# Kernel tuning notes

Measured on AMD Instinct MI355X. Metric: run time of the kernel, lower is better.

Reference implementation:

```python
import jax, jax.numpy as jnp
import numpy as np

IN_DIM = 1024
OUT_DIM = 1024
NUM_EXPERTS = 8
TOP_K = 2
B = 8192


def setup_inputs() -> dict:
    key = jax.random.key(0)
    ks = jax.random.split(key, 8)
    s_in = 1.0 / np.sqrt(IN_DIM)
    s_out = 1.0 / np.sqrt(OUT_DIM)
    return {
        "x": jax.random.normal(ks[0], (B, IN_DIM), dtype=jnp.float32),
        # router Linear(in_dim, num_experts)
        "rw": jax.random.uniform(ks[1], (IN_DIM, NUM_EXPERTS), jnp.float32, -s_in, s_in),
        "rb": jax.random.uniform(ks[2], (NUM_EXPERTS,), jnp.float32, -s_in, s_in),
        # expert MLPs stacked along expert axis
        "w1": jax.random.uniform(ks[3], (NUM_EXPERTS, IN_DIM, OUT_DIM), jnp.float32, -s_in, s_in),
        "b1": jax.random.uniform(ks[4], (NUM_EXPERTS, OUT_DIM), jnp.float32, -s_in, s_in),
        "w2": jax.random.uniform(ks[5], (NUM_EXPERTS, OUT_DIM, OUT_DIM), jnp.float32, -s_out, s_out),
        "b2": jax.random.uniform(ks[6], (NUM_EXPERTS, OUT_DIM), jnp.float32, -s_out, s_out),
    }


def reference(x, rw, rb, w1, b1, w2, b2):
    # ---- TopkRouter ----
    logits = x @ rw + rb                                  # [B, E]
    topk_vals, topk_idx = jax.lax.top_k(logits, TOP_K)    # [B, K]
    neg_inf = jnp.full_like(logits, -jnp.inf)
    rows = jnp.arange(logits.shape[0])[:, None]
    sparse_logits = neg_inf.at[rows, topk_idx].set(topk_vals)
    gating = jax.nn.softmax(sparse_logits, axis=-1)       # zeros outside top-k

    # ---- experts: dense compute, gating weights are exactly 0 for
    # non-selected experts so the weighted combine matches the masked
    # dispatch of the original module. ----
    h = jax.nn.relu(jnp.einsum('bi,eio->beo', x, w1) + b1[None])   # [B, E, out]
    y = jnp.einsum('beh,eho->beo', h, w2) + b2[None]               # [B, E, out]
    fused = jnp.einsum('beo,be->bo', y, gating)                    # [B, out]
    return fused, gating
```

## Files before the change

kernel.cpp:

```cpp
#include <hip/hip_runtime.h>
#include <hip/hip_bf16.h>
#include <cstdint>
#include <cstddef>

#define IN_DIM 1024
#define OUT_DIM 1024
#define NE 8
#define NTOK 8192
#define MT_TILES 20

typedef __bf16 bf16x8 __attribute__((ext_vector_type(8)));
typedef float f32x4 __attribute__((ext_vector_type(4)));
typedef unsigned short ushort8v __attribute__((ext_vector_type(8)));

__device__ __forceinline__ unsigned short f2bf(float f) {
    unsigned u = __float_as_uint(f);
    unsigned r = 0x7fffu + ((u >> 16) & 1u);
    return (unsigned short)((u + r) >> 16);
}

__device__ __forceinline__ void bf2x(unsigned u, float& lo, float& hi) {
    lo = __uint_as_float(u << 16);
    hi = __uint_as_float(u & 0xffff0000u);
}

__device__ __forceinline__ void async16(void* lds, const void* g) {
    __builtin_amdgcn_global_load_lds(
        (const __attribute__((address_space(1))) unsigned int*)g,
        (__attribute__((address_space(3))) unsigned int*)lds,
        16, 0, 0);
}

__global__ __launch_bounds__(256) void convert_transpose_kernel(
    const float* __restrict__ w1, const float* __restrict__ w2,
    unsigned short* __restrict__ w1T, unsigned short* __restrict__ w2T) {
    __shared__ float tile[64][69];
    int z = blockIdx.z;
    const float* src = (z < 8) ? (w1 + (size_t)z * IN_DIM * OUT_DIM)
                               : (w2 + (size_t)(z - 8) * OUT_DIM * OUT_DIM);
    unsigned short* dst = (z < 8) ? (w1T + (size_t)z * IN_DIM * OUT_DIM)
                                  : (w2T + (size_t)(z - 8) * OUT_DIM * OUT_DIM);
    int kt = blockIdx.x * 64, nt = blockIdx.y * 64;
    int t = threadIdx.x;
    int r = t >> 2, cq = (t & 3) * 16;
#pragma unroll
    for (int q = 0; q < 4; ++q) {
        float4 v = *(const float4*)(src + (size_t)(kt + r) * 1024 + nt + cq + q * 4);
        tile[r][cq + q * 4 + 0] = v.x;
        tile[r][cq + q * 4 + 1] = v.y;
        tile[r][cq + q * 4 + 2] = v.z;
        tile[r][cq + q * 4 + 3] = v.w;
    }
    __syncthreads();
    int n2 = t >> 3, k8 = (t & 7) * 8;
#pragma unroll
    for (int q = 0; q < 2; ++q) {
        int n = n2 + q * 32;
        ushort8v o;
#pragma unroll
        for (int i = 0; i < 8; ++i) o[i] = f2bf(tile[k8 + i][n]);
        *(ushort8v*)(dst + (size_t)(nt + n) * 1024 + kt + k8) = o;
    }
}

__global__ __launch_bounds__(256) void router_kernel(
    const float* __restrict__ x, const float* __restrict__ rw,
    const float* __restrict__ rb,
    unsigned short* __restrict__ xb,
    float* __restrict__ gating, int* __restrict__ enc,
    float2* __restrict__ gw, int* __restrict__ cnt) {
    __shared__ float srw[NE * IN_DIM];
    int t = threadIdx.x;
    if (blockIdx.x == 0 && t < NE) cnt[t] = 0;
#pragma unroll
    for (int i = 0; i < 4; ++i) {
        int k = t + i * 256;
        float4 a = *(const float4*)(rw + (size_t)k * NE);
        float4 b = *(const float4*)(rw + (size_t)k * NE + 4);
        srw[0 * IN_DIM + k] = a.x; srw[1 * IN_DIM + k] = a.y;
        srw[2 * IN_DIM + k] = a.z; srw[3 * IN_DIM + k] = a.w;
        srw[4 * IN_DIM + k] = b.x; srw[5 * IN_DIM + k] = b.y;
        srw[6 * IN_DIM + k] = b.z; srw[7 * IN_DIM + k] = b.w;
    }
    __syncthreads();
    int wave = t >> 6, lane = t & 63;
    int tok = blockIdx.x * 4 + wave;
    const float* xrow = x + (size_t)tok * IN_DIM;
    unsigned short* xbrow = xb + (size_t)tok * IN_DIM;
    float acc[NE] = {0, 0, 0, 0, 0, 0, 0, 0};
#pragma unroll
    for (int i = 0; i < 4; ++i) {
        int k = i * 256 + lane * 4;
        float4 xv = *(const float4*)(xrow + k);
        ushort4 o;
        o.x = f2bf(xv.x); o.y = f2bf(xv.y); o.z = f2bf(xv.z); o.w = f2bf(xv.w);
        *(ushort4*)(xbrow + k) = o;
#pragma unroll
        for (int e = 0; e < NE; ++e) {
            float4 wv = *(const float4*)(srw + e * IN_DIM + k);
            acc[e] = fmaf(xv.x, wv.x, fmaf(xv.y, wv.y, fmaf(xv.z, wv.z, fmaf(xv.w, wv.w, acc[e]))));
        }
    }
#pragma unroll
    for (int e = 0; e < NE; ++e) {
#pragma unroll
        for (int off = 32; off > 0; off >>= 1) acc[e] += __shfl_xor(acc[e], off);
        acc[e] += rb[e];
    }
    int e0 = 0; float v0 = acc[0];
#pragma unroll
    for (int e = 1; e < NE; ++e) if (acc[e] > v0) { v0 = acc[e]; e0 = e; }
    int e1 = -1; float v1 = -3.4e38f;
#pragma unroll
    for (int e = 0; e < NE; ++e) if (e != e0 && acc[e] > v1) { v1 = acc[e]; e1 = e; }
    float tg = __expf(v1 - v0);
    float inv = 1.0f / (1.0f + tg);
    float g0 = inv, g1 = tg * inv;
    if (lane < NE) gating[(size_t)tok * NE + lane] = (lane == e0) ? g0 : ((lane == e1) ? g1 : 0.0f);
    if (lane == 0) {
        enc[tok] = e0 | (e1 << 8);
        gw[tok] = make_float2(g0, g1);
    }
}

__global__ __launch_bounds__(256) void bucket_kernel(
    const int* __restrict__ enc,
    int* __restrict__ bidx, int* __restrict__ slots, int* __restrict__ cnt) {
    int tok = blockIdx.x * 256 + threadIdx.x;
    int lane = threadIdx.x & 63;
    int v = enc[tok];
    int e0 = v & 0xff, e1 = (v >> 8) & 0xff;
    unsigned long long below = (1ull << lane) - 1ull;
    int p0 = 0, p1 = 0;
#pragma unroll
    for (int e = 0; e < NE; ++e) {
        unsigned long long m0 = __ballot(e0 == e);
        unsigned long long m1 = __ballot(e1 == e);
        int c0 = __popcll(m0), c1 = __popcll(m1);
        int base = 0;
        if (lane == 0 && (c0 + c1)) base = atomicAdd(&cnt[e], c0 + c1);
        base = __shfl(base, 0);
        if (e0 == e) p0 = base + __popcll(m0 & below);
        if (e1 == e) p1 = base + c0 + __popcll(m1 & below);
    }
    bidx[e0 * NTOK + p0] = tok;
    bidx[e1 * NTOK + p1] = tok;
    slots[2 * tok + 0] = (e0 << 13) | p0;
    slots[2 * tok + 1] = (e1 << 13) | p1;
}

__device__ __forceinline__ int prefix_cnt(const int* __restrict__ cnt, int e) {
    int s = 0;
    for (int i = 0; i < NE; ++i) s += (i < e) ? cnt[i] : 0;
    return s;
}

__device__ __forceinline__ void kstep(const unsigned short* Ab,
                                      const unsigned short* Bb,
                                      f32x4 (&acc)[4][4], int wm, int wn,
                                      int lhalf, int slot) {
    bf16x8 av[4], bv[4];
#pragma unroll
    for (int i = 0; i < 4; ++i)
        av[i] = *(const bf16x8*)(Ab + (wm * 32 + i * 8 + lhalf) * 64 + slot);
#pragma unroll
    for (int j = 0; j < 4; ++j)
        bv[j] = *(const bf16x8*)(Bb + (wn * 32 + j * 8 + lhalf) * 64 + slot);
#pragma unroll
    for (int i = 0; i < 4; ++i)
#pragma unroll
        for (int j = 0; j < 4; ++j)
            acc[i][j] = __builtin_amdgcn_mfma_f32_16x16x32_bf16(av[i], bv[j], acc[i][j], 0, 0, 0);
}


__global__ __launch_bounds__(256) void gemm1_kernel(
    const unsigned short* __restrict__ xb, const unsigned short* __restrict__ w1T,
    const float* __restrict__ b1, const int* __restrict__ bidx,
    const int* __restrict__ cnt,
    unsigned short* __restrict__ H) {
    int b = blockIdx.x;
    int e = b & 7;
    int t2 = b >> 3;
    int nt = t2 & 7;
    int mt = t2 >> 3;
    int n_e = cnt[e];
    if (mt * 128 >= n_e) return;
    __shared__ __attribute__((aligned(16))) unsigned short As[3][64 * 64];
    __shared__ __attribute__((aligned(16))) unsigned short Bs[3][64 * 64];
    int t = threadIdx.x, wave = t >> 6, lane = t & 63;
    const int* be = bidx + e * NTOK;
    const unsigned short* agp[2]; const unsigned short* bgp[2];
    int ldsoff[2];
#pragma unroll
    for (int is = 0; is < 2; ++is) {
        int c = is * 256 + t;
        int line = c >> 3;
        int chunkg = (c & 7) ^ (line & 7);
        int sub = chunkg >> 2;
        int growl = 2 * line + sub;
        int growlB = (line >> 5) * 64 + (line & 7) * 8 + sub * 4 + ((line >> 3) & 3);
        int gcol = (chunkg & 3) * 8;
        int gra = mt * 128 + growl;
        int grac = gra < n_e ? gra : n_e - 1;
        agp[is] = xb + (size_t)be[grac] * IN_DIM + gcol;
        bgp[is] = w1T + ((size_t)e * OUT_DIM + nt * 128 + growlB) * IN_DIM + gcol;
        ldsoff[is] = (is * 256 + wave * 64) * 8;
    }
    int wm = wave & 1, wn = wave >> 1;
    int quad = lane >> 4, l15 = lane & 15;
    int lhalf = l15 >> 1;
    int slot = (((l15 & 1) * 4 + quad) ^ lhalf) * 8;
    f32x4 zero4 = {0.f, 0.f, 0.f, 0.f};
    f32x4 acc[4][4];
#pragma unroll
    for (int i = 0; i < 4; ++i)
#pragma unroll
        for (int j = 0; j < 4; ++j) acc[i][j] = zero4;

#pragma unroll
    for (int pt = 0; pt < 2; ++pt)
#pragma unroll
        for (int is = 0; is < 2; ++is) {
            async16(&As[pt][ldsoff[is]], agp[is] + pt * 32);
            async16(&Bs[pt][ldsoff[is]], bgp[is] + pt * 32);
        }
    int cb = 0, sb = 2;
    for (int it = 0; it < 31; ++it) {
        asm volatile("s_waitcnt vmcnt(4)\n\ts_barrier" ::: "memory");
        if (it < 30) {
            int ktn = (it + 2) * 32;
#pragma unroll
            for (int is = 0; is < 2; ++is) {
                async16(&As[sb][ldsoff[is]], agp[is] + ktn);
                async16(&Bs[sb][ldsoff[is]], bgp[is] + ktn);
            }
        }
        kstep(As[cb], Bs[cb], acc, wm, wn, lhalf, slot);
        cb = (cb == 2) ? 0 : cb + 1;
        sb = (sb == 2) ? 0 : sb + 1;
    }
    asm volatile("s_waitcnt vmcnt(0)\n\ts_barrier" ::: "memory");
    kstep(As[cb], Bs[cb], acc, wm, wn, lhalf, slot);

    int hbase = prefix_cnt(cnt, e);
    const float* b1e = b1 + (size_t)e * OUT_DIM;
    int n0 = nt * 128 + wn * 64 + l15 * 4;
    float4 bias = *(const float4*)(b1e + n0);
#pragma unroll
    for (int i = 0; i < 4; ++i) {
        int m0 = mt * 128 + wm * 64 + i * 16 + quad * 4;
#pragma unroll
        for (int r = 0; r < 4; ++r) {
            int gm = m0 + r;
            if (gm < n_e) {
                float h0 = acc[i][0][r] + bias.x; h0 = h0 > 0.f ? h0 : 0.f;
                float h1 = acc[i][1][r] + bias.y; h1 = h1 > 0.f ? h1 : 0.f;
                float h2 = acc[i][2][r] + bias.z; h2 = h2 > 0.f ? h2 : 0.f;
                float h3 = acc[i][3][r] + bias.w; h3 = h3 > 0.f ? h3 : 0.f;
                ushort4 o;
                o.x = f2bf(h0); o.y = f2bf(h1); o.z = f2bf(h2); o.w = f2bf(h3);
                *(ushort4*)(H + (size_t)(hbase + gm) * OUT_DIM + n0) = o;
            }
        }
    }
}

__global__ __launch_bounds__(256) void gemm2_kernel(
    const unsigned short* __restrict__ H, const unsigned short* __restrict__ w2T,
    const int* __restrict__ cnt,
    unsigned short* __restrict__ Y) {
    int b = blockIdx.x;
    int e = b & 7;
    int t2 = b >> 3;
    int nt = t2 & 7;
    int mt = t2 >> 3;
    int n_e = cnt[e];
    if (mt * 128 >= n_e) return;
    __shared__ __attribute__((aligned(16))) unsigned short As[3][64 * 64];
    __shared__ __attribute__((aligned(16))) unsigned short Bs[3][64 * 64];
    int t = threadIdx.x, wave = t >> 6, lane = t & 63;
    int hbase = prefix_cnt(cnt, e);
    const unsigned short* agp[2]; const unsigned short* bgp[2];
    int ldsoff[2];
#pragma unroll
    for (int is = 0; is < 2; ++is) {
        int c = is * 256 + t;
        int line = c >> 3;
        int chunkg = (c & 7) ^ (line & 7);
        int sub = chunkg >> 2;
        int growl = 2 * line + sub;
        int growlB = (line >> 5) * 64 + (line & 7) * 8 + sub * 4 + ((line >> 3) & 3);
        int gcol = (chunkg & 3) * 8;
        int gra = mt * 128 + growl;
        int grac = gra < n_e ? gra : n_e - 1;
        agp[is] = H + (size_t)(hbase + grac) * OUT_DIM + gcol;
        bgp[is] = w2T + ((size_t)e * OUT_DIM + nt * 128 + growlB) * OUT_DIM + gcol;
        ldsoff[is] = (is * 256 + wave * 64) * 8;
    }
    int wm = wave & 1, wn = wave >> 1;
    int quad = lane >> 4, l15 = lane & 15;
    int lhalf = l15 >> 1;
    int slot = (((l15 & 1) * 4 + quad) ^ lhalf) * 8;
    f32x4 zero4 = {0.f, 0.f, 0.f, 0.f};
    f32x4 acc[4][4];
#pragma unroll
    for (int i = 0; i < 4; ++i)
#pragma unroll
        for (int j = 0; j < 4; ++j) acc[i][j] = zero4;

#pragma unroll
    for (int pt = 0; pt < 2; ++pt)
#pragma unroll
        for (int is = 0; is < 2; ++is) {
            async16(&As[pt][ldsoff[is]], agp[is] + pt * 32);
            async16(&Bs[pt][ldsoff[is]], bgp[is] + pt * 32);
        }
    int cb = 0, sb = 2;
    for (int it = 0; it < 31; ++it) {
        asm volatile("s_waitcnt vmcnt(4)\n\ts_barrier" ::: "memory");
        if (it < 30) {
            int ktn = (it + 2) * 32;
#pragma unroll
            for (int is = 0; is < 2; ++is) {
                async16(&As[sb][ldsoff[is]], agp[is] + ktn);
                async16(&Bs[sb][ldsoff[is]], bgp[is] + ktn);
            }
        }
        kstep(As[cb], Bs[cb], acc, wm, wn, lhalf, slot);
        cb = (cb == 2) ? 0 : cb + 1;
        sb = (sb == 2) ? 0 : sb + 1;
    }
    asm volatile("s_waitcnt vmcnt(0)\n\ts_barrier" ::: "memory");
    kstep(As[cb], Bs[cb], acc, wm, wn, lhalf, slot);

    int n0 = nt * 128 + wn * 64 + l15 * 4;
#pragma unroll
    for (int i = 0; i < 4; ++i) {
        int m0 = mt * 128 + wm * 64 + i * 16 + quad * 4;
#pragma unroll
        for (int r = 0; r < 4; ++r) {
            int gm = m0 + r;
            if (gm < n_e) {
                ushort4 o;
                o.x = f2bf(acc[i][0][r]); o.y = f2bf(acc[i][1][r]);
                o.z = f2bf(acc[i][2][r]); o.w = f2bf(acc[i][3][r]);
                *(ushort4*)(Y + (size_t)(hbase + gm) * OUT_DIM + n0) = o;
            }
        }
    }
}

__global__ __launch_bounds__(256) void combine_kernel(
    const unsigned short* __restrict__ Y, const float* __restrict__ b2,
    const float2* __restrict__ gw, const int* __restrict__ slots,
    const int* __restrict__ cnt, float* __restrict__ out) {
    int t = threadIdx.x, wave = t >> 6, lane = t & 63;
    int tok = blockIdx.x * 4 + wave;
    int pre[NE];
    {
        int s = 0;
#pragma unroll
        for (int i = 0; i < NE; ++i) { pre[i] = s; s += cnt[i]; }
    }
    int s0 = slots[2 * tok], s1 = slots[2 * tok + 1];
    int e0 = s0 >> 13, e1 = s1 >> 13;
    int r0 = pre[e0] + (s0 & 8191);
    int r1 = pre[e1] + (s1 & 8191);
    float2 g = gw[tok];
    const unsigned short* y0 = Y + (size_t)r0 * OUT_DIM;
    const unsigned short* y1 = Y + (size_t)r1 * OUT_DIM;
    const float* c0 = b2 + (size_t)e0 * OUT_DIM;
    const float* c1 = b2 + (size_t)e1 * OUT_DIM;
    float* orow = out + (size_t)tok * OUT_DIM;
#pragma unroll
    for (int i = 0; i < 2; ++i) {
        int c = i * 512 + lane * 8;
        uint4 ua = *(const uint4*)(y0 + c);
        uint4 ub = *(const uint4*)(y1 + c);
        float a[8], b[8];
        bf2x(ua.x, a[0], a[1]); bf2x(ua.y, a[2], a[3]);
        bf2x(ua.z, a[4], a[5]); bf2x(ua.w, a[6], a[7]);
        bf2x(ub.x, b[0], b[1]); bf2x(ub.y, b[2], b[3]);
        bf2x(ub.z, b[4], b[5]); bf2x(ub.w, b[6], b[7]);
        float4 p0 = *(const float4*)(c0 + c);
        float4 p1 = *(const float4*)(c0 + c + 4);
        float4 q0 = *(const float4*)(c1 + c);
        float4 q1 = *(const float4*)(c1 + c + 4);
        float o[8];
        o[0] = g.x * (a[0] + p0.x) + g.y * (b[0] + q0.x);
        o[1] = g.x * (a[1] + p0.y) + g.y * (b[1] + q0.y);
        o[2] = g.x * (a[2] + p0.z) + g.y * (b[2] + q0.z);
        o[3] = g.x * (a[3] + p0.w) + g.y * (b[3] + q0.w);
        o[4] = g.x * (a[4] + p1.x) + g.y * (b[4] + q1.x);
        o[5] = g.x * (a[5] + p1.y) + g.y * (b[5] + q1.y);
        o[6] = g.x * (a[6] + p1.z) + g.y * (b[6] + q1.z);
        o[7] = g.x * (a[7] + p1.w) + g.y * (b[7] + q1.w);
        *(float4*)(orow + c) = make_float4(o[0], o[1], o[2], o[3]);
        *(float4*)(orow + c + 4) = make_float4(o[4], o[5], o[6], o[7]);
    }
}

extern "C" void kernel_launch(void* const* d_in, const int* in_sizes, int n_in,
                              void* d_out, int out_size, void* d_ws, size_t ws_size,
                              hipStream_t stream) {
    const float* x  = (const float*)d_in[0];
    const float* rw = (const float*)d_in[1];
    const float* rb = (const float*)d_in[2];
    const float* w1 = (const float*)d_in[3];
    const float* b1 = (const float*)d_in[4];
    const float* w2 = (const float*)d_in[5];
    const float* b2 = (const float*)d_in[6];
    float* out = (float*)d_out;
    float* gating = out + (size_t)NTOK * OUT_DIM;

    char* ws = (char*)d_ws;
    unsigned short* xb  = (unsigned short*)(ws + 0);
    unsigned short* Y   = (unsigned short*)(ws + 0);
    unsigned short* w1T = (unsigned short*)(ws + 16777216);
    unsigned short* w2T = (unsigned short*)(ws + 33554432);
    unsigned short* H   = (unsigned short*)(ws + 50331648);
    int*   bidx  = (int*)(ws + 83886080);
    int*   slots = (int*)(ws + 84148224);
    int*   cnt   = (int*)(ws + 84213760);
    int*    enc  = (int*)(ws + 84213888);
    float2* gw   = (float2*)(ws + 84246656);

    convert_transpose_kernel<<<dim3(16, 16, 16), 256, 0, stream>>>(w1, w2, w1T, w2T);
    router_kernel<<<NTOK / 4, 256, 0, stream>>>(x, rw, rb, xb, gating, enc, gw, cnt);
    bucket_kernel<<<NTOK / 256, 256, 0, stream>>>(enc, bidx, slots, cnt);
    gemm1_kernel<<<8 * 8 * MT_TILES, 256, 0, stream>>>(xb, w1T, b1, bidx, cnt, H);
    gemm2_kernel<<<8 * 8 * MT_TILES, 256, 0, stream>>>(H, w2T, cnt, Y);
    combine_kernel<<<NTOK / 4, 256, 0, stream>>>(Y, b2, gw, slots, cnt, out);
    (void)in_sizes; (void)n_in; (void)out_size; (void)ws_size;
}
```

Baseline: 294.6 us.

## Fuse combine into gemm2 epilogue via gated atomic adds to output

Removes the separate combine kernel and the bf16 Y intermediate. The gemm2 epilogue now adds bias, multiplies by the gate weight, and atomically accumulates straight into the zeroed fp32 output. Each bidx entry carries a flag bit telling which of the token's two gate weights applies. This drops the Y write and re-read plus one launch, but adds a memset of the output and 2x scattered scalar fp32 atomics, which can be slow and make the summation order nondeterministic.

```diff
diff --git a/kernel.cpp b/kernel.cpp
--- a/kernel.cpp
+++ b/kernel.cpp
@@ -17,11 +17,6 @@
     unsigned u = __float_as_uint(f);
     unsigned r = 0x7fffu + ((u >> 16) & 1u);
     return (unsigned short)((u + r) >> 16);
-}
-
-__device__ __forceinline__ void bf2x(unsigned u, float& lo, float& hi) {
-    lo = __uint_as_float(u << 16);
-    hi = __uint_as_float(u & 0xffff0000u);
 }
 
 __device__ __forceinline__ void async16(void* lds, const void* g) {
@@ -125,7 +120,7 @@
 
 __global__ __launch_bounds__(256) void bucket_kernel(
     const int* __restrict__ enc,
-    int* __restrict__ bidx, int* __restrict__ slots, int* __restrict__ cnt) {
+    int* __restrict__ bidx, int* __restrict__ cnt) {
     int tok = blockIdx.x * 256 + threadIdx.x;
     int lane = threadIdx.x & 63;
     int v = enc[tok];
@@ -144,9 +139,7 @@
         if (e1 == e) p1 = base + c0 + __popcll(m1 & below);
     }
     bidx[e0 * NTOK + p0] = tok;
-    bidx[e1 * NTOK + p1] = tok;
-    slots[2 * tok + 0] = (e0 << 13) | p0;
-    slots[2 * tok + 1] = (e1 << 13) | p1;
+    bidx[e1 * NTOK + p1] = tok | 0x8000;
 }
 
 __device__ __forceinline__ int prefix_cnt(const int* __restrict__ cnt, int e) {
@@ -203,7 +196,7 @@
         int gcol = (chunkg & 3) * 8;
         int gra = mt * 128 + growl;
         int grac = gra < n_e ? gra : n_e - 1;
-        agp[is] = xb + (size_t)be[grac] * IN_DIM + gcol;
+        agp[is] = xb + (size_t)(be[grac] & 0x7fff) * IN_DIM + gcol;
         bgp[is] = w1T + ((size_t)e * OUT_DIM + nt * 128 + growlB) * IN_DIM + gcol;
         ldsoff[is] = (is * 256 + wave * 64) * 8;
     }
@@ -268,8 +261,9 @@
 
 __global__ __launch_bounds__(256) void gemm2_kernel(
     const unsigned short* __restrict__ H, const unsigned short* __restrict__ w2T,
-    const int* __restrict__ cnt,
-    unsigned short* __restrict__ Y) {
+    const float* __restrict__ b2, const int* __restrict__ bidx,
+    const float2* __restrict__ gw, const int* __restrict__ cnt,
+    float* __restrict__ out) {
     int b = blockIdx.x;
     int e = b & 7;
     int t2 = b >> 3;
@@ -335,6 +329,9 @@
     kstep(As[cb], Bs[cb], acc, wm, wn, lhalf, slot);
 
     int n0 = nt * 128 + wn * 64 + l15 * 4;
+    const float* b2e = b2 + (size_t)e * OUT_DIM;
+    float4 bias = *(const float4*)(b2e + n0);
+    const int* be = bidx + e * NTOK;
 #pragma unroll
     for (int i = 0; i < 4; ++i) {
         int m0 = mt * 128 + wm * 64 + i * 16 + quad * 4;
@@ -342,62 +339,17 @@
         for (int r = 0; r < 4; ++r) {
             int gm = m0 + r;
             if (gm < n_e) {
-                ushort4 o;
-                o.x = f2bf(acc[i][0][r]); o.y = f2bf(acc[i][1][r]);
-                o.z = f2bf(acc[i][2][r]); o.w = f2bf(acc[i][3][r]);
-                *(ushort4*)(Y + (size_t)(hbase + gm) * OUT_DIM + n0) = o;
+                int v = be[gm];
+                int tok = v & 0x7fff;
+                float2 g2 = gw[tok];
+                float g = (v >> 15) ? g2.y : g2.x;
+                float* orow = out + (size_t)tok * OUT_DIM + n0;
+                atomicAdd(orow + 0, g * (acc[i][0][r] + bias.x));
+                atomicAdd(orow + 1, g * (acc[i][1][r] + bias.y));
+                atomicAdd(orow + 2, g * (acc[i][2][r] + bias.z));
+                atomicAdd(orow + 3, g * (acc[i][3][r] + bias.w));
             }
         }
-    }
-}
-
-__global__ __launch_bounds__(256) void combine_kernel(
-    const unsigned short* __restrict__ Y, const float* __restrict__ b2,
-    const float2* __restrict__ gw, const int* __restrict__ slots,
-    const int* __restrict__ cnt, float* __restrict__ out) {
-    int t = threadIdx.x, wave = t >> 6, lane = t & 63;
-    int tok = blockIdx.x * 4 + wave;
-    int pre[NE];
-    {
-        int s = 0;
-#pragma unroll
-        for (int i = 0; i < NE; ++i) { pre[i] = s; s += cnt[i]; }
-    }
-    int s0 = slots[2 * tok], s1 = slots[2 * tok + 1];
-    int e0 = s0 >> 13, e1 = s1 >> 13;
-    int r0 = pre[e0] + (s0 & 8191);
-    int r1 = pre[e1] + (s1 & 8191);
-    float2 g = gw[tok];
-    const unsigned short* y0 = Y + (size_t)r0 * OUT_DIM;
-    const unsigned short* y1 = Y + (size_t)r1 * OUT_DIM;
-    const float* c0 = b2 + (size_t)e0 * OUT_DIM;
-    const float* c1 = b2 + (size_t)e1 * OUT_DIM;
-    float* orow = out + (size_t)tok * OUT_DIM;
-#pragma unroll
-    for (int i = 0; i < 2; ++i) {
-        int c = i * 512 + lane * 8;
-        uint4 ua = *(const uint4*)(y0 + c);
-        uint4 ub = *(const uint4*)(y1 + c);
-        float a[8], b[8];
-        bf2x(ua.x, a[0], a[1]); bf2x(ua.y, a[2], a[3]);
-        bf2x(ua.z, a[4], a[5]); bf2x(ua.w, a[6], a[7]);
-        bf2x(ub.x, b[0], b[1]); bf2x(ub.y, b[2], b[3]);
-        bf2x(ub.z, b[4], b[5]); bf2x(ub.w, b[6], b[7]);
-        float4 p0 = *(const float4*)(c0 + c);
-        float4 p1 = *(const float4*)(c0 + c + 4);
-        float4 q0 = *(const float4*)(c1 + c);
-        float4 q1 = *(const float4*)(c1 + c + 4);
-        float o[8];
-        o[0] = g.x * (a[0] + p0.x) + g.y * (b[0] + q0.x);
-        o[1] = g.x * (a[1] + p0.y) + g.y * (b[1] + q0.y);
-        o[2] = g.x * (a[2] + p0.z) + g.y * (b[2] + q0.z);
-        o[3] = g.x * (a[3] + p0.w) + g.y * (b[3] + q0.w);
-        o[4] = g.x * (a[4] + p1.x) + g.y * (b[4] + q1.x);
-        o[5] = g.x * (a[5] + p1.y) + g.y * (b[5] + q1.y);
-        o[6] = g.x * (a[6] + p1.z) + g.y * (b[6] + q1.z);
-        o[7] = g.x * (a[7] + p1.w) + g.y * (b[7] + q1.w);
-        *(float4*)(orow + c) = make_float4(o[0], o[1], o[2], o[3]);
-        *(float4*)(orow + c + 4) = make_float4(o[4], o[5], o[6], o[7]);
     }
 }
 
@@ -416,21 +368,19 @@
 
     char* ws = (char*)d_ws;
     unsigned short* xb  = (unsigned short*)(ws + 0);
-    unsigned short* Y   = (unsigned short*)(ws + 0);
     unsigned short* w1T = (unsigned short*)(ws + 16777216);
     unsigned short* w2T = (unsigned short*)(ws + 33554432);
     unsigned short* H   = (unsigned short*)(ws + 50331648);
     int*   bidx  = (int*)(ws + 83886080);
-    int*   slots = (int*)(ws + 84148224);
     int*   cnt   = (int*)(ws + 84213760);
     int*    enc  = (int*)(ws + 84213888);
     float2* gw   = (float2*)(ws + 84246656);
 
+    hipMemsetAsync(out, 0, (size_t)NTOK * OUT_DIM * sizeof(float), stream);
     convert_transpose_kernel<<<dim3(16, 16, 16), 256, 0, stream>>>(w1, w2, w1T, w2T);
     router_kernel<<<NTOK / 4, 256, 0, stream>>>(x, rw, rb, xb, gating, enc, gw, cnt);
-    bucket_kernel<<<NTOK / 256, 256, 0, stream>>>(enc, bidx, slots, cnt);
+    bucket_kernel<<<NTOK / 256, 256, 0, stream>>>(enc, bidx, cnt);
     gemm1_kernel<<<8 * 8 * MT_TILES, 256, 0, stream>>>(xb, w1T, b1, bidx, cnt, H);
-    gemm2_kernel<<<8 * 8 * MT_TILES, 256, 0, stream>>>(H, w2T, cnt, Y);
-    combine_kernel<<<NTOK / 4, 256, 0, stream>>>(Y, b2, gw, slots, cnt, out);
+    gemm2_kernel<<<8 * 8 * MT_TILES, 256, 0, stream>>>(H, w2T, b2, bidx, gw, cnt, out);
     (void)in_sizes; (void)n_in; (void)out_size; (void)ws_size;
 }
```

Result: slower. 484.3 us (+64.4%).
